# Kernel tuning notes

Hardware: AMD Instinct MI355X
Metric: run time of the kernel (lower is better)

Reference implementation:

```python
import jax, jax.numpy as jnp
import numpy as np

N_NODES = 20000   # graph nodes (rows of x)
N_EDGES = 40000
NUM_ENT = 300000  # node_count: embedding table rows
EMB_DIM = 64
D = 2 * EMB_DIM           # self.emb_dim = 128
SE = int(0.36 * D)        # s_emb_dim = 46
TE = D - SE               # t_emb_dim = 82
F = 256                   # raw feature cols of x
HID = 128                 # n_hidden
OUT = 2


def setup_inputs() -> dict:
    key = jax.random.key(0)
    ks = jax.random.split(key, 24)
    def nrm(k, shape, fan_in):
        return jax.random.normal(k, shape, jnp.float32) / np.sqrt(fan_in)
    inp = {
        'x': jax.random.normal(ks[0], (N_NODES, F), jnp.float32),
        'heads': jax.random.randint(ks[1], (N_EDGES,), 0, NUM_ENT),
        'rels': jax.random.randint(ks[2], (N_EDGES,), 0, 4),
        'tails': jax.random.randint(ks[3], (N_EDGES,), 0, NUM_ENT),
        'weeks': jax.random.uniform(ks[4], (N_EDGES,), jnp.float32),
        'edge_src': jnp.sort(jax.random.randint(ks[5], (N_EDGES,), 0, N_NODES)),
        'edge_dst': jax.random.randint(ks[6], (N_EDGES,), 0, N_NODES),
        'node_type': jax.random.randint(ks[7], (N_NODES,), 0, 5),
        'edge_type': jax.random.randint(ks[8], (N_EDGES,), 0, 4),
        'edge_index': jax.random.randint(ks[9], (2, N_EDGES), 0, N_NODES),
        # learned parameters
        'ent_embs': nrm(ks[10], (NUM_ENT, SE), SE),
        'rel_embs': nrm(ks[11], (4, D), D),
        'w_freq': nrm(ks[12], (NUM_ENT, TE), TE),
        'w_phi': nrm(ks[13], (NUM_ENT, TE), TE),
        'w_amp': nrm(ks[14], (NUM_ENT, TE), TE),
        'Wih': nrm(ks[15], (4 * D, D), D),
        'Whh': nrm(ks[16], (4 * D, D), D),
        'bih': jnp.zeros((4 * D,), jnp.float32),
        'bhh': jnp.zeros((4 * D,), jnp.float32),
        'fc1_w': nrm(ks[17], (HID, F + D), F + D),
        'fc1_b': jnp.zeros((HID,), jnp.float32),
        'ln_g': jnp.ones((HID,), jnp.float32),
        'ln_b': jnp.zeros((HID,), jnp.float32),
        'out_w': nrm(ks[18], (OUT, HID), HID),
        'out_b': jnp.zeros((OUT,), jnp.float32),
    }
    return inp


def _lstm_last_per_segment(pre, seg, Whh, bhh):
    """Run one LSTM over edges sorted by seg, resetting state at group
    boundaries; return per-step hidden states and the scatter index that
    selects the last step of each group (others map to dummy row N_NODES).
    pre: [E, 4D] precomputed x @ Wih^T + bih (sorted by seg)."""
    reset = jnp.concatenate([jnp.ones((1,), bool), seg[1:] != seg[:-1]])
    def step(carry, inp):
        h, c = carry
        p, r = inp
        h = jnp.where(r, 0.0, h)
        c = jnp.where(r, 0.0, c)
        gates = p + h @ Whh.T + bhh
        i, f, g, o = jnp.split(gates, 4, axis=-1)
        c = jax.nn.sigmoid(f) * c + jax.nn.sigmoid(i) * jnp.tanh(g)
        h = jax.nn.sigmoid(o) * jnp.tanh(c)
        return (h, c), h
    zero = jnp.zeros((D,), pre.dtype)
    _, hs = jax.lax.scan(step, (zero, zero), (pre, reset))
    is_last = jnp.concatenate([seg[1:] != seg[:-1], jnp.ones((1,), bool)])
    idx = jnp.where(is_last, seg, N_NODES)  # dummy row for non-last steps
    return hs, idx


def reference(x, heads, rels, tails, weeks, edge_src, edge_dst, node_type,
              edge_type, edge_index, ent_embs, rel_embs, w_freq, w_phi, w_amp,
              Wih, Whh, bih, bhh, fc1_w, fc1_b, ln_g, ln_b, out_w, out_b):
    week = weeks.reshape(-1, 1)  # [E,1]
    # getEmbeddings: static entity emb + diachronic (amp*sin(freq*t+phi)) part
    h_t = w_amp[heads] * jnp.sin(w_freq[heads] * week + w_phi[heads])
    t_t = w_amp[tails] * jnp.sin(w_freq[tails] * week + w_phi[tails])
    h = jnp.concatenate([ent_embs[heads], h_t], axis=1)  # [E, D]
    t = jnp.concatenate([ent_embs[tails], t_t], axis=1)  # [E, D]
    r = rel_embs[rels]                                    # [E, D]
    scores = h * r * t                                    # [E, D]

    # Ragged per-group LSTM (src groups, then dst groups overwrite), fused
    # as a single segment-reset scan per pass. Input projection hoisted.
    pre = scores @ Wih.T + bih  # [E, 4D]
    emb = jnp.zeros((N_NODES + 1, D), scores.dtype)
    perm_s = jnp.argsort(edge_src)  # stable
    hs, idx = _lstm_last_per_segment(pre[perm_s], edge_src[perm_s], Whh, bhh)
    emb = emb.at[idx].set(hs)
    perm_d = jnp.argsort(edge_dst)
    hs, idx = _lstm_last_per_segment(pre[perm_d], edge_dst[perm_d], Whh, bhh)
    emb = emb.at[idx].set(hs)
    emb = emb[:N_NODES]

    # (hgtconv2 omitted: GeneralConv source unavailable; treated as identity)
    xc = jnp.concatenate([x, emb], axis=1)  # mask = arange(N): all rows
    h1 = xc @ fc1_w.T + fc1_b
    mu = jnp.mean(h1, axis=-1, keepdims=True)
    var = jnp.mean((h1 - mu) ** 2, axis=-1, keepdims=True)
    h1 = (h1 - mu) / jnp.sqrt(var + 1e-5) * ln_g + ln_b
    h1 = jax.nn.relu(h1)  # dropout: eval mode, identity
    return h1 @ out_w.T + out_b
```

## Files before the change

### kernel.cpp

```cpp
#include <hip/hip_runtime.h>
#include <math.h>

#define N_NODES 20000
#define N_EDGES 40000
#define SE 46
#define TE 82
#define NBLK 79

typedef short  s16x8 __attribute__((ext_vector_type(8)));
typedef short  s16x4 __attribute__((ext_vector_type(4)));
typedef float  f32x4 __attribute__((ext_vector_type(4)));

__device__ __forceinline__ float sigf(float x){ return 1.0f/(1.0f+__expf(-x)); }
__device__ __forceinline__ float tanh_f(float x){ return 1.0f - 2.0f/(__expf(2.0f*x)+1.0f); }
__device__ __forceinline__ int perm_out(int i){ return (i&3)*128 + (i>>2); }
__device__ __forceinline__ unsigned short f2bf(float f){
  unsigned u = __builtin_bit_cast(unsigned, f);
  unsigned r = (u + 0x7fff + ((u>>16)&1)) >> 16;
  return (unsigned short)r;
}
__device__ __forceinline__ float bf2f(short s){
  unsigned u = ((unsigned)(unsigned short)s) << 16;
  return __builtin_bit_cast(float, u);
}

#define GATHER_BLKS 2500
#define PREP_BLKS   704
#define HIST_BLKS   157
#define FRONT_BLKS  (GATHER_BLKS + PREP_BLKS + HIST_BLKS)

__global__ __launch_bounds__(256) void k_front(
    const int* __restrict__ heads, const int* __restrict__ rels,
    const int* __restrict__ tails, const float* __restrict__ weeks,
    const float* __restrict__ ent, const float* __restrict__ rel_embs,
    const float* __restrict__ wfreq, const float* __restrict__ wphi,
    const float* __restrict__ wamp, short* __restrict__ scores,
    const float* __restrict__ Wih, const float* __restrict__ Whh,
    const float* __restrict__ fc1w,
    short* __restrict__ WihB, short* __restrict__ WhhB2, short* __restrict__ fc1wbf,
    const int* __restrict__ esrc, const int* __restrict__ edst,
    int* __restrict__ scnt, int* __restrict__ dcnt){
  int blk = blockIdx.x, tid = threadIdx.x;
  if (blk < GATHER_BLKS){
    int c = blk*256 + tid;
    int e = c >> 4, d0 = (c & 15) << 3;
    int hd = heads[e], tl = tails[e], rl = rels[e];
    float wk = weeks[e];
    float hv[8], tv[8];
    if (d0 + 8 <= SE){
      const float* hp = ent + (size_t)hd*SE + d0;
      const float* tp = ent + (size_t)tl*SE + d0;
      #pragma unroll
      for (int j=0;j<4;j++){
        float2 a = *(const float2*)(hp + j*2); hv[2*j]=a.x; hv[2*j+1]=a.y;
        float2 b = *(const float2*)(tp + j*2); tv[2*j]=b.x; tv[2*j+1]=b.y;
      }
    } else if (d0 >= 48){
      int dt = d0 - SE;
      const float *hf = wfreq + (size_t)hd*TE + dt, *hp2 = wphi + (size_t)hd*TE + dt, *ha = wamp + (size_t)hd*TE + dt;
      const float *tf = wfreq + (size_t)tl*TE + dt, *tp2 = wphi + (size_t)tl*TE + dt, *ta = wamp + (size_t)tl*TE + dt;
      #pragma unroll
      for (int j=0;j<4;j++){
        float2 f_h = *(const float2*)(hf + j*2);
        float2 p_h = *(const float2*)(hp2 + j*2);
        float2 a_h = *(const float2*)(ha + j*2);
        float2 f_t = *(const float2*)(tf + j*2);
        float2 p_t = *(const float2*)(tp2 + j*2);
        float2 a_t = *(const float2*)(ta + j*2);
        hv[2*j]   = a_h.x*__sinf(f_h.x*wk + p_h.x);
        hv[2*j+1] = a_h.y*__sinf(f_h.y*wk + p_h.y);
        tv[2*j]   = a_t.x*__sinf(f_t.x*wk + p_t.x);
        tv[2*j+1] = a_t.y*__sinf(f_t.y*wk + p_t.y);
      }
    } else {
      #pragma unroll
      for (int j=0;j<8;j++){
        int d = 40 + j;
        if (d < SE){
          hv[j] = ent[(size_t)hd*SE + d];
          tv[j] = ent[(size_t)tl*SE + d];
        } else {
          int dt = d - SE;
          hv[j] = wamp[(size_t)hd*TE+dt]*__sinf(wfreq[(size_t)hd*TE+dt]*wk + wphi[(size_t)hd*TE+dt]);
          tv[j] = wamp[(size_t)tl*TE+dt]*__sinf(wfreq[(size_t)tl*TE+dt]*wk + wphi[(size_t)tl*TE+dt]);
        }
      }
    }
    const float* rp = rel_embs + rl*128 + d0;
    float4 r0 = *(const float4*)rp, r1 = *(const float4*)(rp+4);
    float rv[8] = {r0.x,r0.y,r0.z,r0.w, r1.x,r1.y,r1.z,r1.w};
    s16x8 o;
    #pragma unroll
    for (int j=0;j<8;j++) o[j] = (short)f2bf(hv[j]*rv[j]*tv[j]);
    *(s16x8*)(scores + (size_t)e*128 + d0) = o;
  } else if (blk < GATHER_BLKS + PREP_BLKS){
    int idx = (blk - GATHER_BLKS)*256 + tid;
    if (idx < 65536){
      int i = idx >> 7, k = idx & 127;
      WihB[idx] = (short)f2bf(Wih[perm_out(i)*128 + k]);
    } else if (idx < 131072){
      int j = idx - 65536;
      WhhB2[j] = (short)f2bf(Whh[j]);
    } else if (idx < 180224){
      int j = idx - 131072;
      fc1wbf[j] = (short)f2bf(fc1w[j]);
    }
  } else {
    int e = (blk - GATHER_BLKS - PREP_BLKS)*256 + tid;
    if (e < N_EDGES){ atomicAdd(&scnt[esrc[e]],1); atomicAdd(&dcnt[edst[e]],1); }
  }
}

__global__ __launch_bounds__(256) void k_pgscan(
    const short* __restrict__ scores, const short* __restrict__ WihB,
    const float* __restrict__ bih, const float* __restrict__ bhh,
    short* __restrict__ pre2b,
    const int* __restrict__ scnt, const int* __restrict__ dcnt,
    int* __restrict__ sstart, int* __restrict__ dstart){
  __shared__ char As[32*256];
  __shared__ char Bs[32*1024];
  __shared__ int wsA[4];
  int blk = blockIdx.x, tid = threadIdx.x;
  if (blk < 2){
    const int* cnt = blk ? dcnt : scnt;
    int* start = blk ? dstart : sstart;
    int base = tid*79;
    int lim = min(base+79, N_NODES);
    int tsum = 0;
    for (int i=base;i<lim;i++) tsum += cnt[i];
    int lane = tid & 63, wv4 = tid >> 6;
    int incl = tsum;
    #pragma unroll
    for (int m=1;m<64;m<<=1){ int u = __shfl_up(incl, m); if (lane >= m) incl += u; }
    if (lane == 63) wsA[wv4] = incl;
    __syncthreads();
    int woff = 0;
    for (int k=0;k<wv4;k++) woff += wsA[k];
    int run = woff + incl - tsum;
    for (int i=base;i<lim;i++){ start[i] = run; run += cnt[i]; }
    if (tid == 255) start[N_NODES] = run;
    return;
  }
  int e0 = (blk-2) * 32;
  #pragma unroll
  for (int q=0;q<2;q++){
    int c = tid + 256*q;
    int el = c >> 4, k8 = c & 15;
    s16x8 v = *(const s16x8*)(scores + (size_t)(e0+el)*128 + k8*8);
    *(s16x8*)(As + ((el*256 + k8*16) ^ ((el&7)<<4))) = v;
  }
  __syncthreads();
  int lane = tid & 63, w = tid >> 6;
  int cl = lane & 15, kq = lane >> 4;
  s16x8 a[2][4];
  #pragma unroll
  for (int ks=0;ks<4;ks++){
    int kb = ks*64 + kq*16;
    a[0][ks] = *(const s16x8*)(As + (((cl   )*256 + kb) ^ ((cl&7)<<4)));
    a[1][ks] = *(const s16x8*)(As + (((cl+16)*256 + kb) ^ (((cl+16)&7)<<4)));
  }
  f32x4 D[2][8];
  #pragma unroll
  for (int m=0;m<2;m++)
    #pragma unroll
    for (int i=0;i<8;i++) D[m][i] = (f32x4){0.f,0.f,0.f,0.f};
  #pragma unroll
  for (int i=0;i<8;i++){
    int n = w*128 + i*16 + cl;
    const short* bp = WihB + (size_t)n*128 + kq*8;
    #pragma unroll
    for (int ks=0;ks<4;ks++){
      s16x8 b = *(const s16x8*)(bp + ks*32);
      D[0][i] = __builtin_amdgcn_mfma_f32_16x16x32_bf16(a[0][ks], b, D[0][i], 0, 0, 0);
      D[1][i] = __builtin_amdgcn_mfma_f32_16x16x32_bf16(a[1][ks], b, D[1][i], 0, 0, 0);
    }
  }
  #pragma unroll
  for (int i=0;i<8;i++){
    int n = w*128 + i*16 + cl;
    int pn = perm_out(n);
    float bb = bih[pn] + bhh[pn];
    #pragma unroll
    for (int m=0;m<2;m++){
      #pragma unroll
      for (int q2=0;q2<4;q2++){
        int r = m*16 + kq*4 + q2;
        *(short*)(Bs + ((r*1024 + n*2) ^ ((r&15)<<4))) = (short)f2bf(D[m][i][q2] + bb);
      }
    }
  }
  __syncthreads();
  #pragma unroll
  for (int j=0;j<8;j++){
    int idx = j*256 + tid;
    int r = idx >> 6;
    int cb = (idx & 63) * 16;
    s16x8 v = *(const s16x8*)(Bs + ((r*1024 + cb) ^ ((r&15)<<4)));
    *(s16x8*)(pre2b + (size_t)e0*512 + (size_t)idx*8) = v;
  }
}

__global__ __launch_bounds__(256) void k_scatcb1(
    const int* __restrict__ edst, const int* __restrict__ dstart,
    int* __restrict__ dc2, int* __restrict__ dlist,
    const int* __restrict__ sstart, int* __restrict__ bhist){
  int blk = blockIdx.x, tid = threadIdx.x;
  if (blk < HIST_BLKS){
    int e = blk*256 + tid;
    if (e < N_EDGES){
      int d = edst[e]; int p2 = dstart[d] + atomicAdd(&dc2[d],1); dlist[p2]=e;
    }
  } else {
    __shared__ int h[128];
    int b2 = blk - HIST_BLKS;
    if (tid < 128) h[tid] = 0;
    __syncthreads();
    int n = b2*256 + tid;
    if (n < N_NODES){
      int c  = sstart[n+1]-sstart[n];
      int c2 = dstart[n+1]-dstart[n];
      if (c>0 && c2==0) atomicAdd(&h[min(c,63)], 1);
      if (c2>0) atomicAdd(&h[64+min(c2,63)], 1);
    }
    __syncthreads();
    if (tid < 128) bhist[tid*NBLK + b2] = h[tid];
  }
}

__device__ __forceinline__ int mapbin(int s){
  int p = s / (63*NBLK);
  int r = s - p*(63*NBLK);
  int li = r / NBLK;
  int b  = r - li*NBLK;
  int l  = 63 - li;
  return (p*64 + l)*NBLK + b;
}

__global__ __launch_bounds__(256) void k_sortcb2(
    const int* __restrict__ dstart, int* __restrict__ dlist,
    const int* __restrict__ bhist, int* __restrict__ boff,
    int* __restrict__ nchains){
  int blk = blockIdx.x, tid = threadIdx.x;
  __shared__ int wsum[4];
  __shared__ int pend[2];
  if (blk < NBLK){
    int n = blk*256 + tid;
    if (n < N_NODES){
      int a = dstart[n], b = dstart[n+1];
      for (int i=a+1;i<b;i++){
        int v = dlist[i]; int j=i-1;
        while (j>=a && dlist[j]>v){ dlist[j+1]=dlist[j]; j--; }
        dlist[j+1]=v;
      }
    }
  } else {
    const int S = 2*63*NBLK;
    const int CH2 = 39;
    int tsum = 0;
    for (int j=0;j<CH2;j++){
      int s = tid*CH2 + j;
      if (s < S) tsum += bhist[mapbin(s)];
    }
    int lane = tid & 63, wv = tid >> 6;
    int incl = tsum;
    #pragma unroll
    for (int m=1;m<64;m<<=1){ int u = __shfl_up(incl, m); if (lane >= m) incl += u; }
    if (lane==63) wsum[wv] = incl;
    __syncthreads();
    int woff = 0;
    for (int k=0;k<wv;k++) woff += wsum[k];
    int run = woff + incl - tsum;
    for (int j=0;j<CH2;j++){
      int s = tid*CH2 + j;
      if (s < S){
        int bi = mapbin(s);
        int val = bhist[bi];
        boff[bi] = run;
        run += val;
        if (s == 63*NBLK - 1) pend[0] = run;
        if (s == S - 1)       pend[1] = run;
      }
    }
    __syncthreads();
    if (tid == 0){
      nchains[0] = pend[0];
      nchains[1] = pend[1] - pend[0];
    }
  }
}

__global__ void k_cbin3(const int* __restrict__ sstart, const int* __restrict__ dstart,
                        const int* __restrict__ boff, const int* __restrict__ nchains,
                        int* __restrict__ cnode, int* __restrict__ cstart,
                        int* __restrict__ clen, int* __restrict__ degf){
  __shared__ int h[128];
  int tid = threadIdx.x, blk = blockIdx.x;
  if (tid < 128) h[tid] = 0;
  __syncthreads();
  int n = blk*256 + tid;
  int bin0=-1, bin1=-1, r0=0, r1=0, a0=0, c0=0, a1=0, c1=0;
  if (n < N_NODES){
    a0 = sstart[n]; c0 = sstart[n+1]-a0;
    a1 = dstart[n]; c1 = dstart[n+1]-a1;
    degf[n] = (c0+c1 > 0) ? 1 : 0;
    if (c0>0 && c1==0){ bin0 = min(c0,63);    r0 = atomicAdd(&h[bin0], 1); }
    if (c1>0)         { bin1 = 64+min(c1,63); r1 = atomicAdd(&h[bin1], 1); }
  }
  __syncthreads();
  int nch0 = nchains[0];
  if (bin0 >= 0){
    int pos = boff[bin0*NBLK + blk] + r0;
    cnode[pos] = n; cstart[pos] = a0; clen[pos] = c0;
  }
  if (bin1 >= 0){
    int pos = boff[bin1*NBLK + blk] + r1 - nch0;
    cnode[N_NODES+pos] = n; cstart[N_NODES+pos] = a1; clen[N_NODES+pos] = c1;
  }
}

__global__ __launch_bounds__(512, 1) void k_lstm9(
    const short* __restrict__ pre2b, const short* __restrict__ WhhB2,
    const int* __restrict__ cnode, const int* __restrict__ cstart,
    const int* __restrict__ clen, const int* __restrict__ nchains,
    const int* __restrict__ dlist, int* __restrict__ ctr,
    float* __restrict__ emb){
  __shared__ char Hb[2][8192];
  __shared__ int M[193];
  int tid = threadIdx.x;
  int lane = tid & 63, wv = tid >> 6;
  int cl = lane & 15, kq = lane >> 4;
  int d_own = wv*16 + cl;
  s16x8 wf[4][4];
  #pragma unroll
  for (int i=0;i<4;i++)
    #pragma unroll
    for (int ks=0;ks<4;ks++)
      wf[i][ks] = *(const s16x8*)(WhhB2 + (size_t)(i*128 + d_own)*128 + ks*32 + kq*8);
  int nch0 = nchains[0], nch1 = nchains[1];
  int B0 = (nch0+31)>>5, B1 = (nch1+31)>>5;
  while (true){
    if (tid==0) M[192] = atomicAdd(ctr, 1);
    __syncthreads();
    int nb = M[192];
    if (nb >= B0 + B1) break;
    int pass = (nb >= B0) ? 1 : 0;
    int batch = pass ? nb - B0 : nb;
    int b0 = batch << 5;
    int nch = pass ? nch1 : nch0;
    if (tid < 32){
      int j = b0 + tid;
      int valid = (j < nch);
      int ci = pass*N_NODES + j;
      int st = valid ? cstart[ci] : 0;
      int ln = valid ? clen[ci] : 0;
      M[tid] = ln; M[32+tid] = st; M[160+tid] = valid ? cnode[ci] : -1;
      M[64+tid]  = (ln > 0) ? (pass ? dlist[st]   : st  ) : 0;
      M[96+tid]  = (ln > 1) ? (pass ? dlist[st+1] : st+1) : 0;
      M[128+tid] = (ln > 2) ? (pass ? dlist[st+2] : st+2) : 0;
    }
    *(unsigned long long*)(&Hb[0][tid*16])   = 0ull;
    *(unsigned long long*)(&Hb[0][tid*16+8]) = 0ull;
    float cst[8]  = {0.f,0.f,0.f,0.f,0.f,0.f,0.f,0.f};
    float hreg[8] = {0.f,0.f,0.f,0.f,0.f,0.f,0.f,0.f};
    __syncthreads();
    int mylen[8];
    #pragma unroll
    for (int m=0;m<2;m++)
      #pragma unroll
      for (int q=0;q<4;q++) mylen[m*4+q] = M[m*16 + kq*4 + q];
    int ml = 0;
    #pragma unroll 1
    for (int j=0;j<32;j++) ml = max(ml, M[j]);
    s16x4 pvA[8], pvB[8];
    #pragma unroll
    for (int m=0;m<2;m++)
      #pragma unroll
      for (int q=0;q<4;q++){
        int r = m*16 + kq*4 + q;
        pvA[m*4+q] = *(const s16x4*)(pre2b + (size_t)M[64+r]*512 + d_own*4);
        pvB[m*4+q] = *(const s16x4*)(pre2b + (size_t)M[96+r]*512 + d_own*4);
      }
    __syncthreads();
    int cur = 0;
    int sw = 0;
    int s2 = 2;
    for (int t=0; t<ml; t++){
      if (tid < 32){
        int ln = M[tid];
        int nxt = M[32+tid] + t + 3;
        M[64 + (sw<<5) + tid] = (t+3 < ln) ? (pass ? dlist[nxt] : nxt) : 0;
      }
      s16x4 pvC[8];
      const int* eidN = M + 64 + (s2<<5);
      #pragma unroll
      for (int m=0;m<2;m++)
        #pragma unroll
        for (int q=0;q<4;q++){
          int r = m*16 + kq*4 + q;
          pvC[m*4+q] = *(const s16x4*)(pre2b + (size_t)eidN[r]*512 + d_own*4);
        }
      f32x4 D[2][4];
      #pragma unroll
      for (int m=0;m<2;m++)
        #pragma unroll
        for (int i=0;i<4;i++) D[m][i] = (f32x4){0.f,0.f,0.f,0.f};
      char* Hc = Hb[cur];
      #pragma unroll
      for (int ks=0; ks<4; ks++){
        int kb = ks*64 + kq*16;
        s16x8 a0 = *(const s16x8*)(Hc + (((cl   )*256 + kb) ^ ((cl&7)<<4)));
        s16x8 a1 = *(const s16x8*)(Hc + (((cl+16)*256 + kb) ^ (((cl+16)&7)<<4)));
        #pragma unroll
        for (int i=0;i<4;i++){
          D[0][i] = __builtin_amdgcn_mfma_f32_16x16x32_bf16(a0, wf[i][ks], D[0][i], 0, 0, 0);
          D[1][i] = __builtin_amdgcn_mfma_f32_16x16x32_bf16(a1, wf[i][ks], D[1][i], 0, 0, 0);
        }
      }
      char* Hn = Hb[cur^1];
      #pragma unroll
      for (int m=0;m<2;m++)
        #pragma unroll
        for (int q=0;q<4;q++){
          int r = m*16 + kq*4 + q;
          if (t < mylen[m*4+q]){
            s16x4 p = pvA[m*4+q];
            float gi = D[m][0][q] + bf2f(p[0]);
            float gf = D[m][1][q] + bf2f(p[1]);
            float gg = D[m][2][q] + bf2f(p[2]);
            float go = D[m][3][q] + bf2f(p[3]);
            int idx = m*4+q;
            cst[idx] = sigf(gf)*cst[idx] + sigf(gi)*tanh_f(gg);
            float h = sigf(go)*tanh_f(cst[idx]);
            hreg[idx] = h;
            *(short*)(Hn + ((r*256 + d_own*2) ^ ((r&7)<<4))) = (short)f2bf(h);
          }
        }
      __syncthreads();
      #pragma unroll
      for (int i=0;i<8;i++){ pvA[i] = pvB[i]; pvB[i] = pvC[i]; }
      sw = (sw == 2) ? 0 : sw + 1;
      s2 = (s2 == 2) ? 0 : s2 + 1;
      cur ^= 1;
    }
    #pragma unroll
    for (int m=0;m<2;m++)
      #pragma unroll
      for (int q=0;q<4;q++){
        int r = m*16 + kq*4 + q;
        int n = M[160+r];
        if (mylen[m*4+q] > 0 && n >= 0){
          emb[(size_t)n*128 + d_own] = hreg[m*4+q];
        }
      }
    __syncthreads();
  }
}

__global__ __launch_bounds__(512) void k_mlp2(
    const float* __restrict__ x, const float* __restrict__ emb,
    const int* __restrict__ degf,
    const short* __restrict__ fc1wbf, const float* __restrict__ fc1b,
    const float* __restrict__ lng, const float* __restrict__ lnb,
    const float* __restrict__ outw, const float* __restrict__ outb,
    float* __restrict__ out){
  __shared__ char As[32*768];
  __shared__ float hbuf[32][132];
  int tid = threadIdx.x;
  int lane = tid & 63, w = tid >> 6;
  int base = blockIdx.x * 32;
  #pragma unroll
  for (int q=0;q<3;q++){
    int i = tid + 512*q;
    int r = i / 48, c = i - r*48;
    s16x8 v8 = {0,0,0,0,0,0,0,0};
    if (c < 32){
      const float* src = x + (size_t)(base+r)*256 + c*8;
      float4 v0 = *(const float4*)src;
      float4 v1 = *(const float4*)(src+4);
      v8[0]=(short)f2bf(v0.x); v8[1]=(short)f2bf(v0.y); v8[2]=(short)f2bf(v0.z); v8[3]=(short)f2bf(v0.w);
      v8[4]=(short)f2bf(v1.x); v8[5]=(short)f2bf(v1.y); v8[6]=(short)f2bf(v1.z); v8[7]=(short)f2bf(v1.w);
    } else if (degf[base+r]){
      const float* src = emb + (size_t)(base+r)*128 + (c-32)*8;
      float4 v0 = *(const float4*)src;
      float4 v1 = *(const float4*)(src+4);
      v8[0]=(short)f2bf(v0.x); v8[1]=(short)f2bf(v0.y); v8[2]=(short)f2bf(v0.z); v8[3]=(short)f2bf(v0.w);
      v8[4]=(short)f2bf(v1.x); v8[5]=(short)f2bf(v1.y); v8[6]=(short)f2bf(v1.z); v8[7]=(short)f2bf(v1.w);
    }
    *(s16x8*)(As + ((r*768 + c*16) ^ ((r&7)<<4))) = v8;
  }
  __syncthreads();
  int cl = lane & 15, kq = lane >> 4;
  f32x4 D0 = {0.f,0.f,0.f,0.f}, D1 = {0.f,0.f,0.f,0.f};
  const short* bp = fc1wbf + (size_t)(w*16 + cl)*384 + kq*8;
  #pragma unroll
  for (int ks=0; ks<12; ks++){
    s16x8 b = *(const s16x8*)(bp + ks*32);
    int kb = ks*64 + kq*16;
    s16x8 a0 = *(const s16x8*)(As + (((cl   )*768 + kb) ^ ((cl&7)<<4)));
    s16x8 a1 = *(const s16x8*)(As + (((cl+16)*768 + kb) ^ (((cl+16)&7)<<4)));
    D0 = __builtin_amdgcn_mfma_f32_16x16x32_bf16(a0, b, D0, 0, 0, 0);
    D1 = __builtin_amdgcn_mfma_f32_16x16x32_bf16(a1, b, D1, 0, 0, 0);
  }
  int col = w*16 + cl;
  float bb = fc1b[col];
  #pragma unroll
  for (int q=0;q<4;q++){
    hbuf[kq*4+q][col]    = D0[q] + bb;
    hbuf[16+kq*4+q][col] = D1[q] + bb;
  }
  __syncthreads();
  int sub = lane >> 4, l16 = lane & 15;
  int nd = w*4 + sub;
  float v[8];
  float s = 0.f;
  #pragma unroll
  for (int j=0;j<8;j++){ v[j] = hbuf[nd][l16*8+j]; s += v[j]; }
  #pragma unroll
  for (int m=1;m<16;m<<=1) s += __shfl_xor(s, m);
  float mu = s * (1.f/128.f);
  float va = 0.f;
  #pragma unroll
  for (int j=0;j<8;j++){ float dm = v[j]-mu; va += dm*dm; }
  #pragma unroll
  for (int m=1;m<16;m<<=1) va += __shfl_xor(va, m);
  float rstd = rsqrtf(va*(1.f/128.f) + 1e-5f);
  float o0=0.f, o1=0.f;
  #pragma unroll
  for (int j=0;j<8;j++){
    int c = l16*8+j;
    float h1 = (v[j]-mu)*rstd*lng[c] + lnb[c];
    h1 = fmaxf(h1, 0.f);
    o0 += h1*outw[c]; o1 += h1*outw[128+c];
  }
  #pragma unroll
  for (int m=1;m<16;m<<=1){ o0 += __shfl_xor(o0,m); o1 += __shfl_xor(o1,m); }
  if (l16==0){
    out[(size_t)(base+nd)*2]   = o0 + outb[0];
    out[(size_t)(base+nd)*2+1] = o1 + outb[1];
  }
}

extern "C" void kernel_launch(void* const* d_in, const int* in_sizes, int n_in,
                              void* d_out, int out_size, void* d_ws, size_t ws_size,
                              hipStream_t stream){
  const float* x      = (const float*)d_in[0];
  const int*   heads  = (const int*)d_in[1];
  const int*   rels   = (const int*)d_in[2];
  const int*   tails  = (const int*)d_in[3];
  const float* weeks  = (const float*)d_in[4];
  const int*   esrc   = (const int*)d_in[5];
  const int*   edst   = (const int*)d_in[6];
  const float* ent    = (const float*)d_in[10];
  const float* rel_e  = (const float*)d_in[11];
  const float* wfreq  = (const float*)d_in[12];
  const float* wphi   = (const float*)d_in[13];
  const float* wamp   = (const float*)d_in[14];
  const float* Wih    = (const float*)d_in[15];
  const float* Whh    = (const float*)d_in[16];
  const float* bih    = (const float*)d_in[17];
  const float* bhh    = (const float*)d_in[18];
  const float* fc1w   = (const float*)d_in[19];
  const float* fc1b   = (const float*)d_in[20];
  const float* lng    = (const float*)d_in[21];
  const float* lnb    = (const float*)d_in[22];
  const float* outw   = (const float*)d_in[23];
  const float* outb   = (const float*)d_in[24];
  float* out = (float*)d_out;

  char* ws = (char*)d_ws;
  size_t off = 0;
  auto alloc = [&](size_t bytes){ void* p = ws + off; off += (bytes + 255) & ~(size_t)255; return p; };
  short* pre2b  = (short*)alloc((size_t)N_EDGES*512*2);
  short* scores = (short*)alloc((size_t)N_EDGES*128*2);
  short* WihB   = (short*)alloc(512*128*2);
  short* WhhB2  = (short*)alloc(512*128*2);
  short* fc1wbf = (short*)alloc(128*384*2);
  float* emb    = (float*)alloc((size_t)N_NODES*128*4);
  int* sstart   = (int*)alloc((N_NODES+1)*4);
  int* dstart   = (int*)alloc((N_NODES+1)*4);
  int* zreg     = (int*)alloc((size_t)(3*N_NODES + 3)*4);
  int* scnt = zreg, *dcnt = zreg+N_NODES, *dc2 = zreg+2*N_NODES;
  int* nchains  = zreg + 3*N_NODES;
  int* ctr      = nchains + 2;
  int* bhist    = (int*)alloc((size_t)128*NBLK*4);
  int* boff     = (int*)alloc((size_t)128*NBLK*4);
  int* dlist    = (int*)alloc(N_EDGES*4);
  int* cnode    = (int*)alloc((size_t)2*N_NODES*4);
  int* cstart   = (int*)alloc((size_t)2*N_NODES*4);
  int* clen     = (int*)alloc((size_t)2*N_NODES*4);
  int* degf     = (int*)alloc((size_t)N_NODES*4);

  hipMemsetAsync(zreg, 0, (size_t)(3*N_NODES + 3)*4, stream);

  k_front<<<FRONT_BLKS, 256, 0, stream>>>(heads, rels, tails, weeks, ent, rel_e,
                                          wfreq, wphi, wamp, scores,
                                          Wih, Whh, fc1w, WihB, WhhB2, fc1wbf,
                                          esrc, edst, scnt, dcnt);
  k_pgscan<<<2 + N_EDGES/32, 256, 0, stream>>>(scores, WihB, bih, bhh, pre2b,
                                               scnt, dcnt, sstart, dstart);
  k_scatcb1<<<HIST_BLKS + NBLK, 256, 0, stream>>>(edst, dstart, dc2, dlist, sstart, bhist);
  k_sortcb2<<<NBLK + 1, 256, 0, stream>>>(dstart, dlist, bhist, boff, nchains);
  k_cbin3<<<NBLK, 256, 0, stream>>>(sstart, dstart, boff, nchains, cnode, cstart, clen, degf);
  k_lstm9<<<512, 512, 0, stream>>>(pre2b, WhhB2, cnode, cstart, clen, nchains,
                                   dlist, ctr, emb);
  k_mlp2<<<N_NODES/32, 512, 0, stream>>>(x, emb, degf, fc1wbf, fc1b, lng, lnb, outw, outb, out);
}
```

Measured before the change: 166.8 us.

## Fuse graph binning kernels into one cooperative kernel with grid syncs

Splits the input-projection GEMM into its own kernel and merges the prefix scan, destination scatter, histogram, sort and chain-binning stages into one cooperative kernel that separates phases with grid-wide syncs. This removes three kernel launches and their gaps from the serial preprocessing chain. The cost is grid.sync overhead, and the GEMM kernel no longer overlaps with the scan blocks it used to share a launch with. degf is now computed in the histogram phase instead of the final binning phase.

```diff
diff --git a/kernel.cpp b/kernel.cpp
--- a/kernel.cpp
+++ b/kernel.cpp
@@ -1,5 +1,8 @@
 #include <hip/hip_runtime.h>
+#include <hip/hip_cooperative_groups.h>
 #include <math.h>
+
+namespace cg = cooperative_groups;
 
 #define N_NODES 20000
 #define N_EDGES 40000
@@ -28,6 +31,7 @@
 #define PREP_BLKS   704
 #define HIST_BLKS   157
 #define FRONT_BLKS  (GATHER_BLKS + PREP_BLKS + HIST_BLKS)
+#define BIN_BLKS    236
 
 __global__ __launch_bounds__(256) void k_front(
     const int* __restrict__ heads, const int* __restrict__ rels,
@@ -111,16 +115,92 @@
   }
 }
 
-__global__ __launch_bounds__(256) void k_pgscan(
+__global__ __launch_bounds__(256) void k_pregemm(
     const short* __restrict__ scores, const short* __restrict__ WihB,
     const float* __restrict__ bih, const float* __restrict__ bhh,
-    short* __restrict__ pre2b,
-    const int* __restrict__ scnt, const int* __restrict__ dcnt,
-    int* __restrict__ sstart, int* __restrict__ dstart){
+    short* __restrict__ pre2b){
   __shared__ char As[32*256];
   __shared__ char Bs[32*1024];
-  __shared__ int wsA[4];
   int blk = blockIdx.x, tid = threadIdx.x;
+  int e0 = blk * 32;
+  #pragma unroll
+  for (int q=0;q<2;q++){
+    int c = tid + 256*q;
+    int el = c >> 4, k8 = c & 15;
+    s16x8 v = *(const s16x8*)(scores + (size_t)(e0+el)*128 + k8*8);
+    *(s16x8*)(As + ((el*256 + k8*16) ^ ((el&7)<<4))) = v;
+  }
+  __syncthreads();
+  int lane = tid & 63, w = tid >> 6;
+  int cl = lane & 15, kq = lane >> 4;
+  s16x8 a[2][4];
+  #pragma unroll
+  for (int ks=0;ks<4;ks++){
+    int kb = ks*64 + kq*16;
+    a[0][ks] = *(const s16x8*)(As + (((cl   )*256 + kb) ^ ((cl&7)<<4)));
+    a[1][ks] = *(const s16x8*)(As + (((cl+16)*256 + kb) ^ (((cl+16)&7)<<4)));
+  }
+  f32x4 D[2][8];
+  #pragma unroll
+  for (int m=0;m<2;m++)
+    #pragma unroll
+    for (int i=0;i<8;i++) D[m][i] = (f32x4){0.f,0.f,0.f,0.f};
+  #pragma unroll
+  for (int i=0;i<8;i++){
+    int n = w*128 + i*16 + cl;
+    const short* bp = WihB + (size_t)n*128 + kq*8;
+    #pragma unroll
+    for (int ks=0;ks<4;ks++){
+      s16x8 b = *(const s16x8*)(bp + ks*32);
+      D[0][i] = __builtin_amdgcn_mfma_f32_16x16x32_bf16(a[0][ks], b, D[0][i], 0, 0, 0);
+      D[1][i] = __builtin_amdgcn_mfma_f32_16x16x32_bf16(a[1][ks], b, D[1][i], 0, 0, 0);
+    }
+  }
+  #pragma unroll
+  for (int i=0;i<8;i++){
+    int n = w*128 + i*16 + cl;
+    int pn = perm_out(n);
+    float bb = bih[pn] + bhh[pn];
+    #pragma unroll
+    for (int m=0;m<2;m++){
+      #pragma unroll
+      for (int q2=0;q2<4;q2++){
+        int r = m*16 + kq*4 + q2;
+        *(short*)(Bs + ((r*1024 + n*2) ^ ((r&15)<<4))) = (short)f2bf(D[m][i][q2] + bb);
+      }
+    }
+  }
+  __syncthreads();
+  #pragma unroll
+  for (int j=0;j<8;j++){
+    int idx = j*256 + tid;
+    int r = idx >> 6;
+    int cb = (idx & 63) * 16;
+    s16x8 v = *(const s16x8*)(Bs + ((r*1024 + cb) ^ ((r&15)<<4)));
+    *(s16x8*)(pre2b + (size_t)e0*512 + (size_t)idx*8) = v;
+  }
+}
+
+__device__ __forceinline__ int mapbin(int s){
+  int p = s / (63*NBLK);
+  int r = s - p*(63*NBLK);
+  int li = r / NBLK;
+  int b  = r - li*NBLK;
+  int l  = 63 - li;
+  return (p*64 + l)*NBLK + b;
+}
+
+__global__ __launch_bounds__(256) void k_bin(
+    const int* __restrict__ scnt, const int* __restrict__ dcnt,
+    int* __restrict__ sstart, int* __restrict__ dstart,
+    const int* __restrict__ edst, int* __restrict__ dc2, int* __restrict__ dlist,
+    int* __restrict__ bhist, int* __restrict__ boff, int* __restrict__ nchains,
+    int* __restrict__ cnode, int* __restrict__ cstart, int* __restrict__ clen,
+    int* __restrict__ degf){
+  cg::grid_group grid = cg::this_grid();
+  __shared__ int sm[130];
+  int blk = blockIdx.x, tid = threadIdx.x;
+
   if (blk < 2){
     const int* cnt = blk ? dcnt : scnt;
     int* start = blk ? dstart : sstart;
@@ -132,117 +212,38 @@
     int incl = tsum;
     #pragma unroll
     for (int m=1;m<64;m<<=1){ int u = __shfl_up(incl, m); if (lane >= m) incl += u; }
-    if (lane == 63) wsA[wv4] = incl;
+    if (lane == 63) sm[wv4] = incl;
     __syncthreads();
     int woff = 0;
-    for (int k=0;k<wv4;k++) woff += wsA[k];
+    for (int k=0;k<wv4;k++) woff += sm[k];
     int run = woff + incl - tsum;
     for (int i=base;i<lim;i++){ start[i] = run; run += cnt[i]; }
     if (tid == 255) start[N_NODES] = run;
-    return;
-  }
-  int e0 = (blk-2) * 32;
-  #pragma unroll
-  for (int q=0;q<2;q++){
-    int c = tid + 256*q;
-    int el = c >> 4, k8 = c & 15;
-    s16x8 v = *(const s16x8*)(scores + (size_t)(e0+el)*128 + k8*8);
-    *(s16x8*)(As + ((el*256 + k8*16) ^ ((el&7)<<4))) = v;
-  }
-  __syncthreads();
-  int lane = tid & 63, w = tid >> 6;
-  int cl = lane & 15, kq = lane >> 4;
-  s16x8 a[2][4];
-  #pragma unroll
-  for (int ks=0;ks<4;ks++){
-    int kb = ks*64 + kq*16;
-    a[0][ks] = *(const s16x8*)(As + (((cl   )*256 + kb) ^ ((cl&7)<<4)));
-    a[1][ks] = *(const s16x8*)(As + (((cl+16)*256 + kb) ^ (((cl+16)&7)<<4)));
-  }
-  f32x4 D[2][8];
-  #pragma unroll
-  for (int m=0;m<2;m++)
-    #pragma unroll
-    for (int i=0;i<8;i++) D[m][i] = (f32x4){0.f,0.f,0.f,0.f};
-  #pragma unroll
-  for (int i=0;i<8;i++){
-    int n = w*128 + i*16 + cl;
-    const short* bp = WihB + (size_t)n*128 + kq*8;
-    #pragma unroll
-    for (int ks=0;ks<4;ks++){
-      s16x8 b = *(const s16x8*)(bp + ks*32);
-      D[0][i] = __builtin_amdgcn_mfma_f32_16x16x32_bf16(a[0][ks], b, D[0][i], 0, 0, 0);
-      D[1][i] = __builtin_amdgcn_mfma_f32_16x16x32_bf16(a[1][ks], b, D[1][i], 0, 0, 0);
-    }
-  }
-  #pragma unroll
-  for (int i=0;i<8;i++){
-    int n = w*128 + i*16 + cl;
-    int pn = perm_out(n);
-    float bb = bih[pn] + bhh[pn];
-    #pragma unroll
-    for (int m=0;m<2;m++){
-      #pragma unroll
-      for (int q2=0;q2<4;q2++){
-        int r = m*16 + kq*4 + q2;
-        *(short*)(Bs + ((r*1024 + n*2) ^ ((r&15)<<4))) = (short)f2bf(D[m][i][q2] + bb);
-      }
-    }
-  }
-  __syncthreads();
-  #pragma unroll
-  for (int j=0;j<8;j++){
-    int idx = j*256 + tid;
-    int r = idx >> 6;
-    int cb = (idx & 63) * 16;
-    s16x8 v = *(const s16x8*)(Bs + ((r*1024 + cb) ^ ((r&15)<<4)));
-    *(s16x8*)(pre2b + (size_t)e0*512 + (size_t)idx*8) = v;
-  }
-}
-
-__global__ __launch_bounds__(256) void k_scatcb1(
-    const int* __restrict__ edst, const int* __restrict__ dstart,
-    int* __restrict__ dc2, int* __restrict__ dlist,
-    const int* __restrict__ sstart, int* __restrict__ bhist){
-  int blk = blockIdx.x, tid = threadIdx.x;
+  }
+  grid.sync();
+
   if (blk < HIST_BLKS){
     int e = blk*256 + tid;
     if (e < N_EDGES){
       int d = edst[e]; int p2 = dstart[d] + atomicAdd(&dc2[d],1); dlist[p2]=e;
     }
   } else {
-    __shared__ int h[128];
     int b2 = blk - HIST_BLKS;
-    if (tid < 128) h[tid] = 0;
+    if (tid < 128) sm[tid] = 0;
     __syncthreads();
     int n = b2*256 + tid;
     if (n < N_NODES){
-      int c  = sstart[n+1]-sstart[n];
-      int c2 = dstart[n+1]-dstart[n];
-      if (c>0 && c2==0) atomicAdd(&h[min(c,63)], 1);
-      if (c2>0) atomicAdd(&h[64+min(c2,63)], 1);
-    }
-    __syncthreads();
-    if (tid < 128) bhist[tid*NBLK + b2] = h[tid];
-  }
-}
-
-__device__ __forceinline__ int mapbin(int s){
-  int p = s / (63*NBLK);
-  int r = s - p*(63*NBLK);
-  int li = r / NBLK;
-  int b  = r - li*NBLK;
-  int l  = 63 - li;
-  return (p*64 + l)*NBLK + b;
-}
-
-__global__ __launch_bounds__(256) void k_sortcb2(
-    const int* __restrict__ dstart, int* __restrict__ dlist,
-    const int* __restrict__ bhist, int* __restrict__ boff,
-    int* __restrict__ nchains){
-  int blk = blockIdx.x, tid = threadIdx.x;
-  __shared__ int wsum[4];
-  __shared__ int pend[2];
+      int c0 = sstart[n+1]-sstart[n];
+      int c1 = dstart[n+1]-dstart[n];
+      degf[n] = (c0+c1 > 0) ? 1 : 0;
+      if (c0>0 && c1==0) atomicAdd(&sm[min(c0,63)], 1);
+      if (c1>0) atomicAdd(&sm[64+min(c1,63)], 1);
+    }
+    __syncthreads();
+    if (tid < 128) bhist[tid*NBLK + b2] = sm[tid];
+  }
+  grid.sync();
+
   if (blk < NBLK){
     int n = blk*256 + tid;
     if (n < N_NODES){
@@ -253,7 +254,7 @@
         dlist[j+1]=v;
       }
     }
-  } else {
+  } else if (blk == NBLK){
     const int S = 2*63*NBLK;
     const int CH2 = 39;
     int tsum = 0;
@@ -265,10 +266,10 @@
     int incl = tsum;
     #pragma unroll
     for (int m=1;m<64;m<<=1){ int u = __shfl_up(incl, m); if (lane >= m) incl += u; }
-    if (lane==63) wsum[wv] = incl;
+    if (lane==63) sm[wv] = incl;
     __syncthreads();
     int woff = 0;
-    for (int k=0;k<wv;k++) woff += wsum[k];
+    for (int k=0;k<wv;k++) woff += sm[k];
     int run = woff + incl - tsum;
     for (int j=0;j<CH2;j++){
       int s = tid*CH2 + j;
@@ -277,44 +278,39 @@
         int val = bhist[bi];
         boff[bi] = run;
         run += val;
-        if (s == 63*NBLK - 1) pend[0] = run;
-        if (s == S - 1)       pend[1] = run;
+        if (s == 63*NBLK - 1) sm[8] = run;
+        if (s == S - 1)       sm[9] = run;
       }
     }
     __syncthreads();
     if (tid == 0){
-      nchains[0] = pend[0];
-      nchains[1] = pend[1] - pend[0];
-    }
-  }
-}
-
-__global__ void k_cbin3(const int* __restrict__ sstart, const int* __restrict__ dstart,
-                        const int* __restrict__ boff, const int* __restrict__ nchains,
-                        int* __restrict__ cnode, int* __restrict__ cstart,
-                        int* __restrict__ clen, int* __restrict__ degf){
-  __shared__ int h[128];
-  int tid = threadIdx.x, blk = blockIdx.x;
-  if (tid < 128) h[tid] = 0;
-  __syncthreads();
-  int n = blk*256 + tid;
-  int bin0=-1, bin1=-1, r0=0, r1=0, a0=0, c0=0, a1=0, c1=0;
-  if (n < N_NODES){
-    a0 = sstart[n]; c0 = sstart[n+1]-a0;
-    a1 = dstart[n]; c1 = dstart[n+1]-a1;
-    degf[n] = (c0+c1 > 0) ? 1 : 0;
-    if (c0>0 && c1==0){ bin0 = min(c0,63);    r0 = atomicAdd(&h[bin0], 1); }
-    if (c1>0)         { bin1 = 64+min(c1,63); r1 = atomicAdd(&h[bin1], 1); }
-  }
-  __syncthreads();
-  int nch0 = nchains[0];
-  if (bin0 >= 0){
-    int pos = boff[bin0*NBLK + blk] + r0;
-    cnode[pos] = n; cstart[pos] = a0; clen[pos] = c0;
-  }
-  if (bin1 >= 0){
-    int pos = boff[bin1*NBLK + blk] + r1 - nch0;
-    cnode[N_NODES+pos] = n; cstart[N_NODES+pos] = a1; clen[N_NODES+pos] = c1;
+      nchains[0] = sm[8];
+      nchains[1] = sm[9] - sm[8];
+    }
+  }
+  grid.sync();
+
+  if (blk < NBLK){
+    if (tid < 128) sm[tid] = 0;
+    __syncthreads();
+    int n = blk*256 + tid;
+    int bin0=-1, bin1=-1, r0=0, r1=0, a0=0, c0=0, a1=0, c1=0;
+    if (n < N_NODES){
+      a0 = sstart[n]; c0 = sstart[n+1]-a0;
+      a1 = dstart[n]; c1 = dstart[n+1]-a1;
+      if (c0>0 && c1==0){ bin0 = min(c0,63);    r0 = atomicAdd(&sm[bin0], 1); }
+      if (c1>0)         { bin1 = 64+min(c1,63); r1 = atomicAdd(&sm[bin1], 1); }
+    }
+    __syncthreads();
+    int nch0 = nchains[0];
+    if (bin0 >= 0){
+      int pos = boff[bin0*NBLK + blk] + r0;
+      cnode[pos] = n; cstart[pos] = a0; clen[pos] = c0;
+    }
+    if (bin1 >= 0){
+      int pos = boff[bin1*NBLK + blk] + r1 - nch0;
+      cnode[N_NODES+pos] = n; cstart[N_NODES+pos] = a1; clen[N_NODES+pos] = c1;
+    }
   }
 }
 
@@ -596,11 +592,14 @@
                                           wfreq, wphi, wamp, scores,
                                           Wih, Whh, fc1w, WihB, WhhB2, fc1wbf,
                                           esrc, edst, scnt, dcnt);
-  k_pgscan<<<2 + N_EDGES/32, 256, 0, stream>>>(scores, WihB, bih, bhh, pre2b,
-                                               scnt, dcnt, sstart, dstart);
-  k_scatcb1<<<HIST_BLKS + NBLK, 256, 0, stream>>>(edst, dstart, dc2, dlist, sstart, bhist);
-  k_sortcb2<<<NBLK + 1, 256, 0, stream>>>(dstart, dlist, bhist, boff, nchains);
-  k_cbin3<<<NBLK, 256, 0, stream>>>(sstart, dstart, boff, nchains, cnode, cstart, clen, degf);
+  k_pregemm<<<N_EDGES/32, 256, 0, stream>>>(scores, WihB, bih, bhh, pre2b);
+  {
+    void* args[] = { (void*)&scnt, (void*)&dcnt, (void*)&sstart, (void*)&dstart,
+                     (void*)&edst, (void*)&dc2, (void*)&dlist,
+                     (void*)&bhist, (void*)&boff, (void*)&nchains,
+                     (void*)&cnode, (void*)&cstart, (void*)&clen, (void*)&degf };
+    hipLaunchCooperativeKernel((const void*)k_bin, dim3(BIN_BLKS), dim3(256), args, 0, stream);
+  }
   k_lstm9<<<512, 512, 0, stream>>>(pre2b, WhhB2, cnode, cstart, clen, nchains,
                                    dlist, ctr, emb);
   k_mlp2<<<N_NODES/32, 512, 0, stream>>>(x, emb, degf, fc1wbf, fc1b, lng, lnb, outw, outb, out);
```

Measured after the change: 268.6 us (median of 3 runs). 61.0% more time.
